# Kernel tuning notes

Measured on AMD Instinct MI355X. Metric: run time of the kernel, lower is better.

Reference implementation:

```python
import jax, jax.numpy as jnp
import numpy as np

H = 64          # HIDDEN_DIM
V = 64          # VOCAB_SIZE
LN_EPS = 1e-5   # torch LayerNorm default
D_EPS = 1e-6    # denom epsilon in delta rule
MEM_SCALE = 1.0 # forward default arg


def setup_inputs() -> dict:
    key = jax.random.key(0)
    ks = jax.random.split(key, 8)
    B, L = 16, 2048
    s = lambda k, shape: (jax.random.normal(k, shape, jnp.float32) * 0.05)
    return {
        "seq": jax.random.randint(ks[0], (B, L), 0, V),
        "embed": s(ks[1], (V, H)),
        "W1": s(ks[2], (H, 2 * H)), "b1": jnp.zeros((2 * H,), jnp.float32),
        "W2": s(ks[3], (2 * H, H)), "b2": jnp.zeros((H,), jnp.float32),
        "gamma": jnp.ones((H,), jnp.float32), "beta": jnp.zeros((H,), jnp.float32),
        "Wr": s(ks[4], (H, H)), "br": jnp.zeros((H,), jnp.float32),
        "Wo": s(ks[5], (H, V)), "bo": jnp.zeros((V,), jnp.float32),
    }


def reference(seq, embed, W1, b1, W2, b2, gamma, beta, Wr, br, Wo, bo):
    h = embed[seq]                                  # (B, L, H)
    ff = jax.nn.relu(h @ W1 + b1) @ W2 + b2         # (B, L, H)
    x = h + ff
    mu = x.mean(-1, keepdims=True)
    var = x.var(-1, keepdims=True)                  # biased, as torch LayerNorm
    h = (x - mu) / jnp.sqrt(var + LN_EPS) * gamma + beta

    B = h.shape[0]
    keys = jnp.swapaxes(h[:, :-1, :], 0, 1)         # (L-1, B, H): all but last token

    def step(M, k):                                  # M: (B, H, H), k: (B, H)
        v_pred = jnp.einsum('bij,bj->bi', M, k)
        denom = (k * k).sum(-1, keepdims=True) + D_EPS
        dv = k - v_pred / denom
        M = M + MEM_SCALE * dv[:, :, None] * k[:, None, :]
        return M, None

    M0 = jnp.zeros((B, H, H), h.dtype)
    M, _ = jax.lax.scan(step, M0, keys)

    q = h[:, -1, :]                                  # last token as query
    ctx = jnp.einsum('bij,bj->bi', M, q)             # (B, H)
    return (ctx @ Wr + br) @ Wo + bo                 # (B, V)
```

## Files before the change

### kernel.cpp

```cpp
#include <hip/hip_runtime.h>

#define HDIM 64
#define LSEQ 2048
#define BATCH 16
#define LN_EPS 1e-5f
#define D_EPS 1e-6f
#define NSEG 16
#define CPS 8

typedef unsigned short u16;
typedef unsigned int   u32;

__device__ __forceinline__ float bf2f(u16 v) {
    return __uint_as_float(((u32)v) << 16);
}
__device__ __forceinline__ u16 f2bf(float f) {
    u32 u = __float_as_uint(f);
    return (u16)((u + 0x7FFFu + ((u >> 16) & 1u)) >> 16);
}

#define P_SW1   0
#define P_SW2   33792
#define P_ET    68608
#define P_HIDT  86016
#define P_RED1  120832
#define P_RED2  121888
#define P_SMU   122944
#define P_SRSTD 123216
#define H_ROWS  123488
#define H_INVD  158304
#define SMEM_BYTES 158816
#define C_S     0
#define C_V     17408
#define C_BM    34816
#define C_Z     39168
#define C_GM    43520

__global__ __launch_bounds__(256, 1) void fused_pc_kernel(
    const int* __restrict__ seq, const float* __restrict__ embed,
    const float* __restrict__ W1, const float* __restrict__ b1,
    const float* __restrict__ W2, const float* __restrict__ b2,
    const float* __restrict__ gamma, const float* __restrict__ beta,
    u32* __restrict__ PK, u16* __restrict__ q_ws)
{
    __shared__ __align__(16) char smem[SMEM_BYTES];
    const int t = threadIdx.x;
    const int b = blockIdx.x >> 4;
    const int s = blockIdx.x & 15;
    const int tok0 = 1920 - 128 * s;

    float* hrows  = (float*)(smem + H_ROWS);
    float* invd_l = (float*)(smem + H_INVD);

    {
        float* sW1   = (float*)(smem + P_SW1);
        float* sW2   = (float*)(smem + P_SW2);
        float* eT    = (float*)(smem + P_ET);
        float* hidT  = (float*)(smem + P_HIDT);
        float* red1  = (float*)(smem + P_RED1);
        float* red2  = (float*)(smem + P_RED2);
        float* smu   = (float*)(smem + P_SMU);
        float* srstd = (float*)(smem + P_SRSTD);

        {
            const float4* s1 = (const float4*)W1;
#pragma unroll
            for (int q = 0; q < 8; ++q) {
                const int m = t + 256 * q;
                const int row = m >> 5, col = m & 31;
                *(float4*)&sW1[row * 132 + col * 4] = s1[m];
            }
            const float4* s2 = (const float4*)W2;
#pragma unroll
            for (int q = 0; q < 8; ++q) {
                const int m = t + 256 * q;
                const int row = m >> 4, col = m & 15;
                *(float4*)&sW2[row * 68 + col * 4] = s2[m];
            }
        }

        for (int it = 0; it < 2; ++it) {
            const int g0 = b * LSEQ + tok0 + 64 * it;
            __syncthreads();

            {
                const int tk = t >> 2, p = t & 3;
                const int v = seq[g0 + tk];
                const float* er = embed + v * HDIM + 16 * p;
#pragma unroll
                for (int q = 0; q < 4; ++q) {
                    const float4 ev = *(const float4*)(er + 4 * q);
                    const int d = 16 * p + 4 * q;
                    eT[(d + 0) * 68 + tk] = ev.x;
                    eT[(d + 1) * 68 + tk] = ev.y;
                    eT[(d + 2) * 68 + tk] = ev.z;
                    eT[(d + 3) * 68 + tk] = ev.w;
                }
            }
            __syncthreads();

            const int r = t >> 4;
            const int c = t & 15;

            {
                float acc0[4][4], acc1[4][4];
#pragma unroll
                for (int o = 0; o < 4; ++o) {
                    const float bA = b1[4 * c + o];
                    const float bB = b1[64 + 4 * c + o];
#pragma unroll
                    for (int j = 0; j < 4; ++j) { acc0[j][o] = bA; acc1[j][o] = bB; }
                }
                for (int k = 0; k < 64; ++k) {
                    const float4 ev = *(const float4*)&eT[k * 68 + 4 * r];
                    const float4 wa = *(const float4*)&sW1[k * 132 + 4 * c];
                    const float4 wb = *(const float4*)&sW1[k * 132 + 64 + 4 * c];
                    const float e4[4] = {ev.x, ev.y, ev.z, ev.w};
                    const float a4[4] = {wa.x, wa.y, wa.z, wa.w};
                    const float b4[4] = {wb.x, wb.y, wb.z, wb.w};
#pragma unroll
                    for (int j = 0; j < 4; ++j)
#pragma unroll
                        for (int o = 0; o < 4; ++o) {
                            acc0[j][o] = fmaf(e4[j], a4[o], acc0[j][o]);
                            acc1[j][o] = fmaf(e4[j], b4[o], acc1[j][o]);
                        }
                }
#pragma unroll
                for (int o = 0; o < 4; ++o) {
                    const float4 v0 = make_float4(fmaxf(acc0[0][o], 0.f), fmaxf(acc0[1][o], 0.f),
                                                  fmaxf(acc0[2][o], 0.f), fmaxf(acc0[3][o], 0.f));
                    *(float4*)&hidT[(4 * c + o) * 68 + 4 * r] = v0;
                    const float4 v1 = make_float4(fmaxf(acc1[0][o], 0.f), fmaxf(acc1[1][o], 0.f),
                                                  fmaxf(acc1[2][o], 0.f), fmaxf(acc1[3][o], 0.f));
                    *(float4*)&hidT[(64 + 4 * c + o) * 68 + 4 * r] = v1;
                }
            }
            __syncthreads();

            {
                float acc[4][4];
#pragma unroll
                for (int o = 0; o < 4; ++o) {
                    const float bv = b2[4 * c + o];
#pragma unroll
                    for (int j = 0; j < 4; ++j) acc[j][o] = bv;
                }
                for (int k = 0; k < 128; ++k) {
                    const float4 hv = *(const float4*)&hidT[k * 68 + 4 * r];
                    const float4 wv = *(const float4*)&sW2[k * 68 + 4 * c];
                    const float h4[4] = {hv.x, hv.y, hv.z, hv.w};
                    const float w4[4] = {wv.x, wv.y, wv.z, wv.w};
#pragma unroll
                    for (int j = 0; j < 4; ++j)
#pragma unroll
                        for (int o = 0; o < 4; ++o)
                            acc[j][o] = fmaf(h4[j], w4[o], acc[j][o]);
                }
#pragma unroll
                for (int o = 0; o < 4; ++o) {
                    float4 ex = *(float4*)&eT[(4 * c + o) * 68 + 4 * r];
                    ex.x += acc[0][o];
                    ex.y += acc[1][o];
                    ex.z += acc[2][o];
                    ex.w += acc[3][o];
                    *(float4*)&eT[(4 * c + o) * 68 + 4 * r] = ex;
                }
            }
            __syncthreads();

            {
                const int tk = t & 63, p = t >> 6;
                float sv = 0.f, q = 0.f;
#pragma unroll
                for (int i = 0; i < 16; ++i) {
                    const float x = eT[(16 * p + i) * 68 + tk];
                    sv += x;
                    q = fmaf(x, x, q);
                }
                red1[p * 66 + tk] = sv;
                red2[p * 66 + tk] = q;
            }
            __syncthreads();
            if (t < 64) {
                const float sv = ((red1[0 * 66 + t] + red1[1 * 66 + t]) + (red1[2 * 66 + t] + red1[3 * 66 + t]));
                const float qq = ((red2[0 * 66 + t] + red2[1 * 66 + t]) + (red2[2 * 66 + t] + red2[3 * 66 + t]));
                const float mu  = sv * (1.0f / 64.0f);
                const float var = qq * (1.0f / 64.0f) - mu * mu;
                smu[t]   = mu;
                srstd[t] = 1.0f / sqrtf(var + LN_EPS);
            }
            __syncthreads();

            {
                const int tk = t >> 2, p = t & 3;
                const float mu = smu[tk], rstd = srstd[tk];
                const int lrow = 64 * it + tk;
                float hh = 0.f;
#pragma unroll
                for (int i2 = 0; i2 < 8; ++i2) {
                    const int d = 16 * p + 2 * i2;
                    const float x0 = eT[(d + 0) * 68 + tk];
                    const float x1 = eT[(d + 1) * 68 + tk];
                    const float o0 = (x0 - mu) * rstd * gamma[d + 0] + beta[d + 0];
                    const float o1 = (x1 - mu) * rstd * gamma[d + 1] + beta[d + 1];
                    const u16 r0 = f2bf(o0), r1 = f2bf(o1);
                    const float q0f = bf2f(r0), q1f = bf2f(r1);
                    hh = fmaf(q0f, q0f, hh);
                    hh = fmaf(q1f, q1f, hh);
                    hrows[lrow * 68 + d]     = q0f;
                    hrows[lrow * 68 + d + 1] = q1f;
                    if (s == 0 && lrow == 127) {
                        q_ws[b * 64 + d]     = r0;
                        q_ws[b * 64 + d + 1] = r1;
                    }
                }
                red1[p * 66 + tk] = hh;
            }
            __syncthreads();
            if (t < 64) {
                const float hh = ((red1[0 * 66 + t] + red1[1 * 66 + t]) + (red1[2 * 66 + t] + red1[3 * 66 + t]));
                invd_l[64 * it + t] = 1.0f / (hh + D_EPS);
            }
        }
    }
    __syncthreads();

    if (s == 0 && t < 64) hrows[127 * 68 + t] = 0.f;

    {
        float* S  = (float*)(smem + C_S);
        float* V  = (float*)(smem + C_V);
        float* Bm = (float*)(smem + C_BM);
        float* Z  = (float*)(smem + C_Z);
        float* Gm = (float*)(smem + C_GM);

        for (int idx = t; idx < 64 * 64; idx += 256) {
            const int m = idx >> 6, n = idx & 63;
            S[m * 68 + n] = (m == n) ? 1.0f : 0.0f;
            V[m * 68 + n] = 0.0f;
        }

        for (int cc = 0; cc < CPS; ++cc) {
            const int base = 127 - 16 * cc;
            __syncthreads();

            {
                const int i = t >> 4, j = t & 15;
                if (i > j) {
                    const float* ra = &hrows[(base - i) * 68];
                    const float* rb = &hrows[(base - j) * 68];
                    float acc = 0.f;
#pragma unroll
                    for (int m = 0; m < 64; m += 4) {
                        const float4 a  = *(const float4*)&ra[m];
                        const float4 bb = *(const float4*)&rb[m];
                        acc += a.x * bb.x + a.y * bb.y + a.z * bb.z + a.w * bb.w;
                    }
                    Gm[i * 17 + j] = acc * invd_l[base - j];
                }
            }
            __syncthreads();

            if (t < 64) {
                const int n = t;
                float Breg[16];
#pragma unroll
                for (int i = 0; i < 16; ++i) {
                    float acc = hrows[(base - i) * 68 + n];
#pragma unroll
                    for (int j = 0; j < 16; ++j)
                        if (j < i) acc = fmaf(-Gm[i * 17 + j], Breg[j], acc);
                    Breg[i] = acc;
                    Bm[i * 68 + n] = acc;
                }
            }
            __syncthreads();

            {
                const int i  = t & 15;
                const int n0 = (t >> 4) * 4;
                float4 z = make_float4(0.f, 0.f, 0.f, 0.f);
#pragma unroll
                for (int mq = 0; mq < 16; ++mq) {
                    const float4 bq = *(const float4*)&Bm[i * 68 + mq * 4];
                    const float4 s0 = *(const float4*)&S[(mq * 4 + 0) * 68 + n0];
                    const float4 s1 = *(const float4*)&S[(mq * 4 + 1) * 68 + n0];
                    const float4 s2 = *(const float4*)&S[(mq * 4 + 2) * 68 + n0];
                    const float4 s3 = *(const float4*)&S[(mq * 4 + 3) * 68 + n0];
                    z.x = fmaf(bq.x, s0.x, fmaf(bq.y, s1.x, fmaf(bq.z, s2.x, fmaf(bq.w, s3.x, z.x))));
                    z.y = fmaf(bq.x, s0.y, fmaf(bq.y, s1.y, fmaf(bq.z, s2.y, fmaf(bq.w, s3.y, z.y))));
                    z.z = fmaf(bq.x, s0.z, fmaf(bq.y, s1.z, fmaf(bq.z, s2.z, fmaf(bq.w, s3.z, z.z))));
                    z.w = fmaf(bq.x, s0.w, fmaf(bq.y, s1.w, fmaf(bq.z, s2.w, fmaf(bq.w, s3.w, z.w))));
                }
                *(float4*)&Z[i * 68 + n0] = z;
            }
            __syncthreads();

            {
                const int n0 = (t & 15) * 4;
                const int mh = t >> 4;
                float iv16[16];
#pragma unroll
                for (int q4 = 0; q4 < 4; ++q4) {
                    const float4 v4 = *(const float4*)&invd_l[base - 15 + 4 * q4];
                    iv16[15 - 4 * q4]     = v4.x;
                    iv16[15 - 4 * q4 - 1] = v4.y;
                    iv16[15 - 4 * q4 - 2] = v4.z;
                    iv16[15 - 4 * q4 - 3] = v4.w;
                }
                float4 sacc[4], vacc[4];
#pragma unroll
                for (int p = 0; p < 4; ++p) {
                    sacc[p] = *(float4*)&S[(mh + 16 * p) * 68 + n0];
                    vacc[p] = *(float4*)&V[(mh + 16 * p) * 68 + n0];
                }
#pragma unroll
                for (int j = 0; j < 16; ++j) {
                    const float4 zq = *(const float4*)&Z[j * 68 + n0];
                    const float iv = iv16[j];
                    float4 ztq;
                    ztq.x = zq.x * iv; ztq.y = zq.y * iv;
                    ztq.z = zq.z * iv; ztq.w = zq.w * iv;
                    const float* kr = &hrows[(base - j) * 68];
                    const float k0 = kr[mh];
                    const float k1 = kr[mh + 16];
                    const float k2 = kr[mh + 32];
                    const float k3 = kr[mh + 48];
                    vacc[0].x = fmaf(k0, zq.x, vacc[0].x); vacc[0].y = fmaf(k0, zq.y, vacc[0].y);
                    vacc[0].z = fmaf(k0, zq.z, vacc[0].z); vacc[0].w = fmaf(k0, zq.w, vacc[0].w);
                    vacc[1].x = fmaf(k1, zq.x, vacc[1].x); vacc[1].y = fmaf(k1, zq.y, vacc[1].y);
                    vacc[1].z = fmaf(k1, zq.z, vacc[1].z); vacc[1].w = fmaf(k1, zq.w, vacc[1].w);
                    vacc[2].x = fmaf(k2, zq.x, vacc[2].x); vacc[2].y = fmaf(k2, zq.y, vacc[2].y);
                    vacc[2].z = fmaf(k2, zq.z, vacc[2].z); vacc[2].w = fmaf(k2, zq.w, vacc[2].w);
                    vacc[3].x = fmaf(k3, zq.x, vacc[3].x); vacc[3].y = fmaf(k3, zq.y, vacc[3].y);
                    vacc[3].z = fmaf(k3, zq.z, vacc[3].z); vacc[3].w = fmaf(k3, zq.w, vacc[3].w);
                    sacc[0].x = fmaf(-k0, ztq.x, sacc[0].x); sacc[0].y = fmaf(-k0, ztq.y, sacc[0].y);
                    sacc[0].z = fmaf(-k0, ztq.z, sacc[0].z); sacc[0].w = fmaf(-k0, ztq.w, sacc[0].w);
                    sacc[1].x = fmaf(-k1, ztq.x, sacc[1].x); sacc[1].y = fmaf(-k1, ztq.y, sacc[1].y);
                    sacc[1].z = fmaf(-k1, ztq.z, sacc[1].z); sacc[1].w = fmaf(-k1, ztq.w, sacc[1].w);
                    sacc[2].x = fmaf(-k2, ztq.x, sacc[2].x); sacc[2].y = fmaf(-k2, ztq.y, sacc[2].y);
                    sacc[2].z = fmaf(-k2, ztq.z, sacc[2].z); sacc[2].w = fmaf(-k2, ztq.w, sacc[2].w);
                    sacc[3].x = fmaf(-k3, ztq.x, sacc[3].x); sacc[3].y = fmaf(-k3, ztq.y, sacc[3].y);
                    sacc[3].z = fmaf(-k3, ztq.z, sacc[3].z); sacc[3].w = fmaf(-k3, ztq.w, sacc[3].w);
                }
#pragma unroll
                for (int p = 0; p < 4; ++p) {
                    *(float4*)&S[(mh + 16 * p) * 68 + n0] = sacc[p];
                    *(float4*)&V[(mh + 16 * p) * 68 + n0] = vacc[p];
                }
            }
        }
        __syncthreads();

        u32* pk = PK + ((size_t)(b * NSEG + s) << 12);
        for (int idx = t; idx < 4096; idx += 256) {
            const int j = idx >> 6, i = idx & 63;
            const u32 sb = ((u32)f2bf(S[i * 68 + j])) << 16;
            const u32 vb = (u32)f2bf(V[i * 68 + j]);
            pk[idx] = sb | vb;
        }
    }
}

__global__ __launch_bounds__(256, 1) void final_kernel(
    const u16* __restrict__ q_ws, const u32* __restrict__ PK,
    const float* __restrict__ Wr, const float* __restrict__ br,
    const float* __restrict__ Wo, const float* __restrict__ bo,
    float* __restrict__ out)
{
    const int b    = blockIdx.x;
    const int t    = threadIdx.x;
    const int lane = t & 63;
    const int p    = t >> 6;

    __shared__ float psum[4][72];
    __shared__ float rl[64];
    __shared__ float cs[64], rs[64];

    rl[lane] = bf2f(q_ws[b * 64 + lane]);

    float ctxp = 0.f;
    u32 cur[16], nxt[16];
    {
        const u32* pk0 = PK + ((size_t)(b * NSEG + 0) << 12);
#pragma unroll
        for (int jj = 0; jj < 16; ++jj)
            cur[jj] = pk0[(p * 16 + jj) * 64 + lane];
    }
    __syncthreads();

    for (int s = 0; s < NSEG; ++s) {
        const int sn = (s + 1 < NSEG) ? s + 1 : s;
        const u32* pkn = PK + ((size_t)(b * NSEG + sn) << 12);
#pragma unroll
        for (int jj = 0; jj < 16; ++jj)
            nxt[jj] = pkn[(p * 16 + jj) * 64 + lane];

        float accr = 0.f;
#pragma unroll
        for (int jj = 0; jj < 16; ++jj) {
            const u32 pv = cur[jj];
            const float Sv = __uint_as_float(pv & 0xFFFF0000u);
            const float Vv = __uint_as_float(pv << 16);
            const float rj = rl[p * 16 + jj];
            accr = fmaf(Sv, rj, accr);
            ctxp = fmaf(Vv, rj, ctxp);
        }
        psum[p][lane] = accr;
        __syncthreads();
        const float rn = (psum[0][lane] + psum[1][lane]) + (psum[2][lane] + psum[3][lane]);
        __syncthreads();
        rl[lane] = rn;

#pragma unroll
        for (int jj = 0; jj < 16; ++jj) cur[jj] = nxt[jj];
    }

    psum[p][lane] = ctxp;
    __syncthreads();
    if (t < 64)
        cs[t] = (psum[0][t] + psum[1][t]) + (psum[2][t] + psum[3][t]);
    __syncthreads();

    float rv = (p == 0) ? br[lane] : 0.f;
#pragma unroll
    for (int i = 0; i < 16; ++i)
        rv = fmaf(cs[p * 16 + i], Wr[(p * 16 + i) * HDIM + lane], rv);
    psum[p][lane] = rv;
    __syncthreads();
    if (t < 64)
        rs[t] = (psum[0][t] + psum[1][t]) + (psum[2][t] + psum[3][t]);
    __syncthreads();

    float ov = (p == 0) ? bo[lane] : 0.f;
#pragma unroll
    for (int i = 0; i < 16; ++i)
        ov = fmaf(rs[p * 16 + i], Wo[(p * 16 + i) * HDIM + lane], ov);
    psum[p][lane] = ov;
    __syncthreads();
    if (t < 64)
        out[(size_t)b * HDIM + t] = (psum[0][t] + psum[1][t]) + (psum[2][t] + psum[3][t]);
}

extern "C" void kernel_launch(void* const* d_in, const int* in_sizes, int n_in,
                              void* d_out, int out_size, void* d_ws, size_t ws_size,
                              hipStream_t stream)
{
    const int*   seq   = (const int*)  d_in[0];
    const float* embed = (const float*)d_in[1];
    const float* W1    = (const float*)d_in[2];
    const float* b1    = (const float*)d_in[3];
    const float* W2    = (const float*)d_in[4];
    const float* b2    = (const float*)d_in[5];
    const float* gamma = (const float*)d_in[6];
    const float* beta  = (const float*)d_in[7];
    const float* Wr    = (const float*)d_in[8];
    const float* br    = (const float*)d_in[9];
    const float* Wo    = (const float*)d_in[10];
    const float* bo    = (const float*)d_in[11];

    u32* pk_ws = (u32*)d_ws;
    u16* q_ws  = (u16*)(pk_ws + (size_t)BATCH * NSEG * 4096);
    float* outp = (float*)d_out;

    hipLaunchKernelGGL(fused_pc_kernel, dim3(BATCH * NSEG), dim3(256), 0, stream,
                       seq, embed, W1, b1, W2, b2, gamma, beta, pk_ws, q_ws);
    hipLaunchKernelGGL(final_kernel, dim3(BATCH), dim3(256), 0, stream,
                       q_ws, pk_ws, Wr, br, Wo, bo, outp);
}
```

Measured before the change: 139.3 us.

## Split sequence into 32 segments, store weights and keys as bf16 for two blocks/CU

Doubles the number of sequence segments per batch (32 segments of 64 tokens instead of 16 of 128), which halves per-block work and doubles the grid. W1, W2, the hidden activations and the normalized key rows are held in shared memory as bf16 rather than fp32, cutting the LDS footprint from about 159KB to about 81KB so that launch_bounds can request two blocks per CU. This adds bf16 rounding of the weights and FFN hidden values, which the reference computes in fp32, and it gives more segment partial results for the later combine step to merge.

New measurement: 139.4 us, median of 2. About the same (+0.1%).

```diff
diff --git a/kernel.cpp b/kernel.cpp
--- a/kernel.cpp
+++ b/kernel.cpp
@@ -5,8 +5,8 @@
 #define BATCH 16
 #define LN_EPS 1e-5f
 #define D_EPS 1e-6f
-#define NSEG 16
-#define CPS 8
+#define NSEG 32
+#define CPS 4
 
 typedef unsigned short u16;
 typedef unsigned int   u32;
@@ -19,24 +19,24 @@
     return (u16)((u + 0x7FFFu + ((u >> 16) & 1u)) >> 16);
 }
 
-#define P_SW1   0
-#define P_SW2   33792
-#define P_ET    68608
-#define P_HIDT  86016
-#define P_RED1  120832
-#define P_RED2  121888
-#define P_SMU   122944
-#define P_SRSTD 123216
-#define H_ROWS  123488
-#define H_INVD  158304
-#define SMEM_BYTES 158816
+#define A_SW1   0
+#define A_SW2   16896
+#define A_ET    34304
+#define A_HIDT  51712
+#define A_RED1  69120
+#define A_RED2  70176
+#define A_SMU   71232
+#define A_SRSTD 71504
+#define H_ROWS  71776
+#define H_INVD  80480
+#define SMEM_BYTES 80736
 #define C_S     0
 #define C_V     17408
 #define C_BM    34816
 #define C_Z     39168
 #define C_GM    43520
 
-__global__ __launch_bounds__(256, 1) void fused_pc_kernel(
+__global__ __launch_bounds__(256, 2) void fused_pc_kernel(
     const int* __restrict__ seq, const float* __restrict__ embed,
     const float* __restrict__ W1, const float* __restrict__ b1,
     const float* __restrict__ W2, const float* __restrict__ b2,
@@ -45,22 +45,22 @@
 {
     __shared__ __align__(16) char smem[SMEM_BYTES];
     const int t = threadIdx.x;
-    const int b = blockIdx.x >> 4;
-    const int s = blockIdx.x & 15;
-    const int tok0 = 1920 - 128 * s;
-
-    float* hrows  = (float*)(smem + H_ROWS);
+    const int b = blockIdx.x >> 5;
+    const int s = blockIdx.x & 31;
+    const int tok0 = 1984 - 64 * s;
+
+    u16*   hrows  = (u16*)(smem + H_ROWS);
     float* invd_l = (float*)(smem + H_INVD);
 
     {
-        float* sW1   = (float*)(smem + P_SW1);
-        float* sW2   = (float*)(smem + P_SW2);
-        float* eT    = (float*)(smem + P_ET);
-        float* hidT  = (float*)(smem + P_HIDT);
-        float* red1  = (float*)(smem + P_RED1);
-        float* red2  = (float*)(smem + P_RED2);
-        float* smu   = (float*)(smem + P_SMU);
-        float* srstd = (float*)(smem + P_SRSTD);
+        u16*   sW1   = (u16*)(smem + A_SW1);
+        u16*   sW2   = (u16*)(smem + A_SW2);
+        float* eT    = (float*)(smem + A_ET);
+        u16*   hidT  = (u16*)(smem + A_HIDT);
+        float* red1  = (float*)(smem + A_RED1);
+        float* red2  = (float*)(smem + A_RED2);
+        float* smu   = (float*)(smem + A_SMU);
+        float* srstd = (float*)(smem + A_SRSTD);
 
         {
             const float4* s1 = (const float4*)W1;
@@ -68,165 +68,164 @@
             for (int q = 0; q < 8; ++q) {
                 const int m = t + 256 * q;
                 const int row = m >> 5, col = m & 31;
-                *(float4*)&sW1[row * 132 + col * 4] = s1[m];
+                const float4 v = s1[m];
+                ushort4 w;
+                w.x = f2bf(v.x); w.y = f2bf(v.y); w.z = f2bf(v.z); w.w = f2bf(v.w);
+                *(ushort4*)&sW1[row * 132 + col * 4] = w;
             }
             const float4* s2 = (const float4*)W2;
 #pragma unroll
             for (int q = 0; q < 8; ++q) {
                 const int m = t + 256 * q;
                 const int row = m >> 4, col = m & 15;
-                *(float4*)&sW2[row * 68 + col * 4] = s2[m];
-            }
-        }
-
-        for (int it = 0; it < 2; ++it) {
-            const int g0 = b * LSEQ + tok0 + 64 * it;
-            __syncthreads();
-
-            {
-                const int tk = t >> 2, p = t & 3;
-                const int v = seq[g0 + tk];
-                const float* er = embed + v * HDIM + 16 * p;
-#pragma unroll
-                for (int q = 0; q < 4; ++q) {
-                    const float4 ev = *(const float4*)(er + 4 * q);
-                    const int d = 16 * p + 4 * q;
-                    eT[(d + 0) * 68 + tk] = ev.x;
-                    eT[(d + 1) * 68 + tk] = ev.y;
-                    eT[(d + 2) * 68 + tk] = ev.z;
-                    eT[(d + 3) * 68 + tk] = ev.w;
-                }
-            }
-            __syncthreads();
-
-            const int r = t >> 4;
-            const int c = t & 15;
-
-            {
-                float acc0[4][4], acc1[4][4];
-#pragma unroll
-                for (int o = 0; o < 4; ++o) {
-                    const float bA = b1[4 * c + o];
-                    const float bB = b1[64 + 4 * c + o];
-#pragma unroll
-                    for (int j = 0; j < 4; ++j) { acc0[j][o] = bA; acc1[j][o] = bB; }
-                }
-                for (int k = 0; k < 64; ++k) {
-                    const float4 ev = *(const float4*)&eT[k * 68 + 4 * r];
-                    const float4 wa = *(const float4*)&sW1[k * 132 + 4 * c];
-                    const float4 wb = *(const float4*)&sW1[k * 132 + 64 + 4 * c];
-                    const float e4[4] = {ev.x, ev.y, ev.z, ev.w};
-                    const float a4[4] = {wa.x, wa.y, wa.z, wa.w};
-                    const float b4[4] = {wb.x, wb.y, wb.z, wb.w};
-#pragma unroll
-                    for (int j = 0; j < 4; ++j)
-#pragma unroll
-                        for (int o = 0; o < 4; ++o) {
-                            acc0[j][o] = fmaf(e4[j], a4[o], acc0[j][o]);
-                            acc1[j][o] = fmaf(e4[j], b4[o], acc1[j][o]);
-                        }
-                }
-#pragma unroll
-                for (int o = 0; o < 4; ++o) {
-                    const float4 v0 = make_float4(fmaxf(acc0[0][o], 0.f), fmaxf(acc0[1][o], 0.f),
-                                                  fmaxf(acc0[2][o], 0.f), fmaxf(acc0[3][o], 0.f));
-                    *(float4*)&hidT[(4 * c + o) * 68 + 4 * r] = v0;
-                    const float4 v1 = make_float4(fmaxf(acc1[0][o], 0.f), fmaxf(acc1[1][o], 0.f),
-                                                  fmaxf(acc1[2][o], 0.f), fmaxf(acc1[3][o], 0.f));
-                    *(float4*)&hidT[(64 + 4 * c + o) * 68 + 4 * r] = v1;
-                }
-            }
-            __syncthreads();
-
-            {
-                float acc[4][4];
-#pragma unroll
-                for (int o = 0; o < 4; ++o) {
-                    const float bv = b2[4 * c + o];
-#pragma unroll
-                    for (int j = 0; j < 4; ++j) acc[j][o] = bv;
-                }
-                for (int k = 0; k < 128; ++k) {
-                    const float4 hv = *(const float4*)&hidT[k * 68 + 4 * r];
-                    const float4 wv = *(const float4*)&sW2[k * 68 + 4 * c];
-                    const float h4[4] = {hv.x, hv.y, hv.z, hv.w};
-                    const float w4[4] = {wv.x, wv.y, wv.z, wv.w};
-#pragma unroll
-                    for (int j = 0; j < 4; ++j)
-#pragma unroll
-                        for (int o = 0; o < 4; ++o)
-                            acc[j][o] = fmaf(h4[j], w4[o], acc[j][o]);
-                }
-#pragma unroll
-                for (int o = 0; o < 4; ++o) {
-                    float4 ex = *(float4*)&eT[(4 * c + o) * 68 + 4 * r];
-                    ex.x += acc[0][o];
-                    ex.y += acc[1][o];
-                    ex.z += acc[2][o];
-                    ex.w += acc[3][o];
-                    *(float4*)&eT[(4 * c + o) * 68 + 4 * r] = ex;
-                }
-            }
-            __syncthreads();
-
-            {
-                const int tk = t & 63, p = t >> 6;
-                float sv = 0.f, q = 0.f;
-#pragma unroll
-                for (int i = 0; i < 16; ++i) {
-                    const float x = eT[(16 * p + i) * 68 + tk];
-                    sv += x;
-                    q = fmaf(x, x, q);
-                }
-                red1[p * 66 + tk] = sv;
-                red2[p * 66 + tk] = q;
-            }
-            __syncthreads();
-            if (t < 64) {
-                const float sv = ((red1[0 * 66 + t] + red1[1 * 66 + t]) + (red1[2 * 66 + t] + red1[3 * 66 + t]));
-                const float qq = ((red2[0 * 66 + t] + red2[1 * 66 + t]) + (red2[2 * 66 + t] + red2[3 * 66 + t]));
-                const float mu  = sv * (1.0f / 64.0f);
-                const float var = qq * (1.0f / 64.0f) - mu * mu;
-                smu[t]   = mu;
-                srstd[t] = 1.0f / sqrtf(var + LN_EPS);
-            }
-            __syncthreads();
-
-            {
-                const int tk = t >> 2, p = t & 3;
-                const float mu = smu[tk], rstd = srstd[tk];
-                const int lrow = 64 * it + tk;
-                float hh = 0.f;
-#pragma unroll
-                for (int i2 = 0; i2 < 8; ++i2) {
-                    const int d = 16 * p + 2 * i2;
-                    const float x0 = eT[(d + 0) * 68 + tk];
-                    const float x1 = eT[(d + 1) * 68 + tk];
-                    const float o0 = (x0 - mu) * rstd * gamma[d + 0] + beta[d + 0];
-                    const float o1 = (x1 - mu) * rstd * gamma[d + 1] + beta[d + 1];
-                    const u16 r0 = f2bf(o0), r1 = f2bf(o1);
-                    const float q0f = bf2f(r0), q1f = bf2f(r1);
-                    hh = fmaf(q0f, q0f, hh);
-                    hh = fmaf(q1f, q1f, hh);
-                    hrows[lrow * 68 + d]     = q0f;
-                    hrows[lrow * 68 + d + 1] = q1f;
-                    if (s == 0 && lrow == 127) {
-                        q_ws[b * 64 + d]     = r0;
-                        q_ws[b * 64 + d + 1] = r1;
+                const float4 v = s2[m];
+                ushort4 w;
+                w.x = f2bf(v.x); w.y = f2bf(v.y); w.z = f2bf(v.z); w.w = f2bf(v.w);
+                *(ushort4*)&sW2[row * 68 + col * 4] = w;
+            }
+        }
+        {
+            const int tk = t >> 2, p = t & 3;
+            const int v = seq[b * LSEQ + tok0 + tk];
+            const float* er = embed + v * HDIM + 16 * p;
+#pragma unroll
+            for (int q = 0; q < 4; ++q) {
+                const float4 ev = *(const float4*)(er + 4 * q);
+                const int d = 16 * p + 4 * q;
+                eT[(d + 0) * 68 + tk] = ev.x;
+                eT[(d + 1) * 68 + tk] = ev.y;
+                eT[(d + 2) * 68 + tk] = ev.z;
+                eT[(d + 3) * 68 + tk] = ev.w;
+            }
+        }
+        __syncthreads();
+
+        const int r = t >> 4;
+        const int c = t & 15;
+
+        {
+            float acc0[4][4], acc1[4][4];
+#pragma unroll
+            for (int o = 0; o < 4; ++o) {
+                const float bA = b1[4 * c + o];
+                const float bB = b1[64 + 4 * c + o];
+#pragma unroll
+                for (int j = 0; j < 4; ++j) { acc0[j][o] = bA; acc1[j][o] = bB; }
+            }
+            for (int k = 0; k < 64; ++k) {
+                const float4  ev = *(const float4*)&eT[k * 68 + 4 * r];
+                const ushort4 wa = *(const ushort4*)&sW1[k * 132 + 4 * c];
+                const ushort4 wb = *(const ushort4*)&sW1[k * 132 + 64 + 4 * c];
+                const float e4[4] = {ev.x, ev.y, ev.z, ev.w};
+                const float a4[4] = {bf2f(wa.x), bf2f(wa.y), bf2f(wa.z), bf2f(wa.w)};
+                const float b4[4] = {bf2f(wb.x), bf2f(wb.y), bf2f(wb.z), bf2f(wb.w)};
+#pragma unroll
+                for (int j = 0; j < 4; ++j)
+#pragma unroll
+                    for (int o = 0; o < 4; ++o) {
+                        acc0[j][o] = fmaf(e4[j], a4[o], acc0[j][o]);
+                        acc1[j][o] = fmaf(e4[j], b4[o], acc1[j][o]);
                     }
-                }
-                red1[p * 66 + tk] = hh;
-            }
-            __syncthreads();
-            if (t < 64) {
-                const float hh = ((red1[0 * 66 + t] + red1[1 * 66 + t]) + (red1[2 * 66 + t] + red1[3 * 66 + t]));
-                invd_l[64 * it + t] = 1.0f / (hh + D_EPS);
-            }
+            }
+#pragma unroll
+            for (int o = 0; o < 4; ++o) {
+                ushort4 v0, v1;
+                v0.x = f2bf(fmaxf(acc0[0][o], 0.f)); v0.y = f2bf(fmaxf(acc0[1][o], 0.f));
+                v0.z = f2bf(fmaxf(acc0[2][o], 0.f)); v0.w = f2bf(fmaxf(acc0[3][o], 0.f));
+                *(ushort4*)&hidT[(4 * c + o) * 68 + 4 * r] = v0;
+                v1.x = f2bf(fmaxf(acc1[0][o], 0.f)); v1.y = f2bf(fmaxf(acc1[1][o], 0.f));
+                v1.z = f2bf(fmaxf(acc1[2][o], 0.f)); v1.w = f2bf(fmaxf(acc1[3][o], 0.f));
+                *(ushort4*)&hidT[(64 + 4 * c + o) * 68 + 4 * r] = v1;
+            }
+        }
+        __syncthreads();
+
+        {
+            float acc[4][4];
+#pragma unroll
+            for (int o = 0; o < 4; ++o) {
+                const float bv = b2[4 * c + o];
+#pragma unroll
+                for (int j = 0; j < 4; ++j) acc[j][o] = bv;
+            }
+            for (int k = 0; k < 128; ++k) {
+                const ushort4 hv = *(const ushort4*)&hidT[k * 68 + 4 * r];
+                const ushort4 wv = *(const ushort4*)&sW2[k * 68 + 4 * c];
+                const float h4[4] = {bf2f(hv.x), bf2f(hv.y), bf2f(hv.z), bf2f(hv.w)};
+                const float w4[4] = {bf2f(wv.x), bf2f(wv.y), bf2f(wv.z), bf2f(wv.w)};
+#pragma unroll
+                for (int j = 0; j < 4; ++j)
+#pragma unroll
+                    for (int o = 0; o < 4; ++o)
+                        acc[j][o] = fmaf(h4[j], w4[o], acc[j][o]);
+            }
+#pragma unroll
+            for (int o = 0; o < 4; ++o) {
+                float4 ex = *(float4*)&eT[(4 * c + o) * 68 + 4 * r];
+                ex.x += acc[0][o];
+                ex.y += acc[1][o];
+                ex.z += acc[2][o];
+                ex.w += acc[3][o];
+                *(float4*)&eT[(4 * c + o) * 68 + 4 * r] = ex;
+            }
+        }
+        __syncthreads();
+
+        {
+            const int tk = t & 63, p = t >> 6;
+            float sv = 0.f, q = 0.f;
+#pragma unroll
+            for (int i = 0; i < 16; ++i) {
+                const float x = eT[(16 * p + i) * 68 + tk];
+                sv += x;
+                q = fmaf(x, x, q);
+            }
+            red1[p * 66 + tk] = sv;
+            red2[p * 66 + tk] = q;
+        }
+        __syncthreads();
+        if (t < 64) {
+            const float sv = ((red1[0 * 66 + t] + red1[1 * 66 + t]) + (red1[2 * 66 + t] + red1[3 * 66 + t]));
+            const float qq = ((red2[0 * 66 + t] + red2[1 * 66 + t]) + (red2[2 * 66 + t] + red2[3 * 66 + t]));
+            const float mu  = sv * (1.0f / 64.0f);
+            const float var = qq * (1.0f / 64.0f) - mu * mu;
+            smu[t]   = mu;
+            srstd[t] = 1.0f / sqrtf(var + LN_EPS);
+        }
+        __syncthreads();
+
+        {
+            const int tk = t >> 2, p = t & 3;
+            const float mu = smu[tk], rstd = srstd[tk];
+            float hh = 0.f;
+#pragma unroll
+            for (int i2 = 0; i2 < 8; ++i2) {
+                const int d = 16 * p + 2 * i2;
+                const float x0 = eT[(d + 0) * 68 + tk];
+                const float x1 = eT[(d + 1) * 68 + tk];
+                const float o0 = (x0 - mu) * rstd * gamma[d + 0] + beta[d + 0];
+                const float o1 = (x1 - mu) * rstd * gamma[d + 1] + beta[d + 1];
+                const u16 r0 = f2bf(o0), r1 = f2bf(o1);
+                const float q0f = bf2f(r0), q1f = bf2f(r1);
+                hh = fmaf(q0f, q0f, hh);
+                hh = fmaf(q1f, q1f, hh);
+                *(u32*)&hrows[tk * 68 + d] = (u32)r0 | ((u32)r1 << 16);
+                if (s == 0 && tk == 63) {
+                    q_ws[b * 64 + d]     = r0;
+                    q_ws[b * 64 + d + 1] = r1;
+                }
+            }
+            red1[p * 66 + tk] = hh;
+        }
+        __syncthreads();
+        if (t < 64) {
+            const float hh = ((red1[0 * 66 + t] + red1[1 * 66 + t]) + (red1[2 * 66 + t] + red1[3 * 66 + t]));
+            invd_l[t] = 1.0f / (hh + D_EPS);
         }
     }
     __syncthreads();
 
-    if (s == 0 && t < 64) hrows[127 * 68 + t] = 0.f;
+    if (s == 0 && t < 64) hrows[63 * 68 + t] = 0;
 
     {
         float* S  = (float*)(smem + C_S);
@@ -242,20 +241,21 @@
         }
 
         for (int cc = 0; cc < CPS; ++cc) {
-            const int base = 127 - 16 * cc;
+            const int base = 63 - 16 * cc;
             __syncthreads();
 
             {
                 const int i = t >> 4, j = t & 15;
                 if (i > j) {
-                    const float* ra = &hrows[(base - i) * 68];
-                    const float* rb = &hrows[(base - j) * 68];
+                    const u16* ra = &hrows[(base - i) * 68];
+                    const u16* rb = &hrows[(base - j) * 68];
                     float acc = 0.f;
 #pragma unroll
                     for (int m = 0; m < 64; m += 4) {
-                        const float4 a  = *(const float4*)&ra[m];
-                        const float4 bb = *(const float4*)&rb[m];
-                        acc += a.x * bb.x + a.y * bb.y + a.z * bb.z + a.w * bb.w;
+                        const ushort4 a4 = *(const ushort4*)&ra[m];
+                        const ushort4 b4 = *(const ushort4*)&rb[m];
+                        acc += bf2f(a4.x) * bf2f(b4.x) + bf2f(a4.y) * bf2f(b4.y)
+                             + bf2f(a4.z) * bf2f(b4.z) + bf2f(a4.w) * bf2f(b4.w);
                     }
                     Gm[i * 17 + j] = acc * invd_l[base - j];
                 }
@@ -267,7 +267,7 @@
                 float Breg[16];
 #pragma unroll
                 for (int i = 0; i < 16; ++i) {
-                    float acc = hrows[(base - i) * 68 + n];
+                    float acc = bf2f(hrows[(base - i) * 68 + n]);
 #pragma unroll
                     for (int j = 0; j < 16; ++j)
                         if (j < i) acc = fmaf(-Gm[i * 17 + j], Breg[j], acc);
@@ -322,11 +322,11 @@
                     float4 ztq;
                     ztq.x = zq.x * iv; ztq.y = zq.y * iv;
                     ztq.z = zq.z * iv; ztq.w = zq.w * iv;
-                    const float* kr = &hrows[(base - j) * 68];
-                    const float k0 = kr[mh];
-                    const float k1 = kr[mh + 16];
-                    const float k2 = kr[mh + 32];
-                    const float k3 = kr[mh + 48];
+                    const u16* kr = &hrows[(base - j) * 68];
+                    const float k0 = bf2f(kr[mh]);
+                    const float k1 = bf2f(kr[mh + 16]);
+                    const float k2 = bf2f(kr[mh + 32]);
+                    const float k3 = bf2f(kr[mh + 48]);
                     vacc[0].x = fmaf(k0, zq.x, vacc[0].x); vacc[0].y = fmaf(k0, zq.y, vacc[0].y);
                     vacc[0].z = fmaf(k0, zq.z, vacc[0].z); vacc[0].w = fmaf(k0, zq.w, vacc[0].w);
                     vacc[1].x = fmaf(k1, zq.x, vacc[1].x); vacc[1].y = fmaf(k1, zq.y, vacc[1].y);
```
